# Kernel optimization log

Measured on AMD Instinct MI355X. Metric: run time of the kernel, lower is better.

## Reference

```python
import jax, jax.numpy as jnp
import numpy as np
import math

B, S, D = 4, 4096, 1024
NUM_HEADS = 8  # hardcoded in the original via `// 8` and view(..., 8, head_dim)
HEAD_DIM = D // NUM_HEADS


def setup_inputs() -> dict:
    key = jax.random.key(0)
    ks = jax.random.split(key, 11)
    s = 1.0 / math.sqrt(D)
    inp = {
        "input_seq": jax.random.normal(ks[0], (B, S, D), dtype=jnp.float32),
        # Linear weights stored as [in, out] (y = x @ W + b), matching nn.Linear math
        "Wq": jax.random.uniform(ks[1], (D, D), jnp.float32, -s, s),
        "bq": jax.random.uniform(ks[2], (D,), jnp.float32, -s, s),
        "Wk": jax.random.uniform(ks[3], (D, D), jnp.float32, -s, s),
        "bk": jax.random.uniform(ks[4], (D,), jnp.float32, -s, s),
        "Wv": jax.random.uniform(ks[5], (D, D), jnp.float32, -s, s),
        "bv": jax.random.uniform(ks[6], (D,), jnp.float32, -s, s),
        "W1": jax.random.uniform(ks[7], (D, D), jnp.float32, -s, s),
        "b1": jax.random.uniform(ks[8], (D,), jnp.float32, -s, s),
        "W2": jax.random.uniform(ks[9], (D, D), jnp.float32, -s, s),
        "b2": jax.random.uniform(ks[10], (D,), jnp.float32, -s, s),
    }
    return inp


def reference(input_seq, Wq, bq, Wk, bk, Wv, bv, W1, b1, W2, b2):
    # QKV projections (query=key=input_seq in self-attention)
    q = input_seq @ Wq + bq  # [B,S,D]
    k = input_seq @ Wk + bk
    v = input_seq @ Wv + bv

    # Faithful to the original: view(B, S, 8, head_dim) with NO transpose,
    # so attention is computed over the 8 heads within each token position.
    q = q.reshape(B, S, NUM_HEADS, HEAD_DIM)
    k = k.reshape(B, S, NUM_HEADS, HEAD_DIM)
    v = v.reshape(B, S, NUM_HEADS, HEAD_DIM)

    # scores[b,s,h,t] = q[b,s,h,:] . k[b,s,t,:] / sqrt(head_dim)  -> [B,S,8,8]
    scores = jnp.einsum("bshd,bstd->bsht", q, k) / jnp.sqrt(jnp.float32(HEAD_DIM))
    # dropout on scores before softmax: identity at inference
    attn_weights = jax.nn.softmax(scores, axis=-1)  # [B,S,8,8]

    out = jnp.einsum("bsht,bstd->bshd", attn_weights, v).reshape(B, S, D)
    # dropout on attn_output: identity at inference

    # FFN: Linear -> ReLU -> Linear (no residual / layernorm in the original)
    ff = jnp.maximum(out @ W1 + b1, 0.0) @ W2 + b2
    return ff, attn_weights
```

## Files before the change

kernel.cpp:

```cpp
#include <hip/hip_runtime.h>
#include <hip/hip_bf16.h>


#define DI __device__ __forceinline__

typedef __bf16 bf16raw;
typedef bf16raw bf16x8 __attribute__((ext_vector_type(8)));
typedef float floatx4 __attribute__((ext_vector_type(4)));

DI unsigned short f2bf(float f) {
    __hip_bfloat16 h = __float2bfloat16(f);
    return *reinterpret_cast<unsigned short*>(&h);
}

DI void async16(unsigned short* lds, const unsigned short* g) {
    __builtin_amdgcn_global_load_lds(
        (const __attribute__((address_space(1))) void*)g,
        (__attribute__((address_space(3))) void*)lds,
        16, 0, 0);
}

template <typename T> DI T cvt_out(float v);
template <> DI float cvt_out<float>(float v) { return v; }
template <> DI unsigned short cvt_out<unsigned short>(float v) { return f2bf(v); }

template <int K, int N, int GX, typename OutT, bool RELU>
__global__ __launch_bounds__(256, 3)
void gemm_bt_kernel(const unsigned short* __restrict__ A,
                    const unsigned short* __restrict__ Bt,
                    const float* __restrict__ bias,
                    OutT* __restrict__ C)
{
    constexpr int BM = 128, BN = 128, BK = 64;
    __shared__ unsigned short As[BM * BK];
    __shared__ unsigned short Bs[BN * BK];

    const int tid  = threadIdx.x;
    const int wave = tid >> 6;
    const int lane = tid & 63;
    const int quad = lane >> 4;
    const int l16  = lane & 15;
    const int sw7  = l16 & 7;

    const int g   = blockIdx.x + GX * blockIdx.y;
    const int xcd = g & 7;
    const int t   = g >> 3;
    const int bx  = t % GX;
    const int by  = t / GX + (gridDim.y >> 3) * xcd;

    const int m0 = by * BM;
    const int n0 = bx * BN;
    const int wm = (wave >> 1) * 64;
    const int wn = (wave & 1) * 64;

    floatx4 acc[4][4];
    const floatx4 zero = {0.f, 0.f, 0.f, 0.f};
#pragma unroll
    for (int i = 0; i < 4; i++)
#pragma unroll
        for (int j = 0; j < 4; j++) acc[i][j] = zero;

    const int rA = lane >> 3;
    const int kA = (((lane & 7) ^ rA) * 8);
    const unsigned short* aBase = A  + (size_t)(m0 + wave * 32 + rA) * K + kA;
    const unsigned short* bBase = Bt + (size_t)(n0 + wave * 32 + rA) * K + kA;
    unsigned short* aD = &As[wave * 2048];
    unsigned short* bD = &Bs[wave * 2048];

    for (int kt = 0; kt < K; kt += BK) {
        __syncthreads();
#pragma unroll
        for (int c = 0; c < 4; c++) {
            async16(aD + c * 512, aBase + c * 8 * K + kt);
            async16(bD + c * 512, bBase + c * 8 * K + kt);
        }
        __syncthreads();

#pragma unroll
        for (int s = 0; s < 2; s++) {
            bf16x8 af[4], bfr[4];
            const int slot = ((s * 4 + quad) ^ sw7) * 8;
#pragma unroll
            for (int i = 0; i < 4; i++)
                af[i] = *reinterpret_cast<const bf16x8*>(
                    &As[(wm + i * 16 + l16) * BK + slot]);
#pragma unroll
            for (int j = 0; j < 4; j++)
                bfr[j] = *reinterpret_cast<const bf16x8*>(
                    &Bs[(wn + j * 16 + l16) * BK + slot]);
#pragma unroll
            for (int i = 0; i < 4; i++)
#pragma unroll
                for (int j = 0; j < 4; j++)
                    acc[i][j] = __builtin_amdgcn_mfma_f32_16x16x32_bf16(
                        af[i], bfr[j], acc[i][j], 0, 0, 0);
        }
    }

#pragma unroll
    for (int j = 0; j < 4; j++) {
        const int col = n0 + wn + j * 16 + l16;
        const float bv = bias[col];
#pragma unroll
        for (int i = 0; i < 4; i++) {
            const int rbase = m0 + wm + i * 16 + quad * 4;
#pragma unroll
            for (int r = 0; r < 4; r++) {
                float v = acc[i][j][r] + bv;
                if (RELU) v = fmaxf(v, 0.f);
                C[(size_t)(rbase + r) * N + col] = cvt_out<OutT>(v);
            }
        }
    }
}

__global__ void cast_f32_to_bf16(const float* __restrict__ src,
                                 unsigned short* __restrict__ dst, int n4) {
    int i = blockIdx.x * blockDim.x + threadIdx.x;
    if (i < n4) {
        float4 v = reinterpret_cast<const float4*>(src)[i];
        ushort4 o = { f2bf(v.x), f2bf(v.y), f2bf(v.z), f2bf(v.w) };
        reinterpret_cast<ushort4*>(dst)[i] = o;
    }
}

struct WPack {
    const float* src[5];
    unsigned short* dst[5];
};
__global__ void transpose_cast_all(WPack p) {
    __shared__ float tile[32][33];
    const float* W = p.src[blockIdx.z];
    unsigned short* Wt = p.dst[blockIdx.z];
    const int n0 = blockIdx.x * 32, k0 = blockIdx.y * 32;
    const int tx = threadIdx.x, ty = threadIdx.y;
#pragma unroll
    for (int i = 0; i < 32; i += 8)
        tile[ty + i][tx] = W[(size_t)(k0 + ty + i) * 1024 + n0 + tx];
    __syncthreads();
#pragma unroll
    for (int i = 0; i < 32; i += 8)
        Wt[(size_t)(n0 + ty + i) * 1024 + k0 + tx] = f2bf(tile[tx][ty + i]);
}

__global__ void concat_bias(const float* __restrict__ bq,
                            const float* __restrict__ bk,
                            const float* __restrict__ bv,
                            float* __restrict__ dst) {
    int i = blockIdx.x * blockDim.x + threadIdx.x;
    const float* s = (i < 1024) ? bq : ((i < 2048) ? bk : bv);
    dst[i] = s[i & 1023];
}

DI float dot8(unsigned a, unsigned b, float acc) {
    union { unsigned u; float f; } al, ah, bl, bh;
    al.u = a << 16; ah.u = a & 0xffff0000u;
    bl.u = b << 16; bh.u = b & 0xffff0000u;
    return acc + al.f * bl.f + ah.f * bh.f;
}

__global__ __launch_bounds__(256)
void attention_kernel(const unsigned short* __restrict__ qkv,
                      unsigned short* __restrict__ out_bf,
                      float* __restrict__ attn_w)
{
    __shared__ unsigned short sqkv[4][3072];
    __shared__ float sw[4][64];
    const int tid  = threadIdx.x;
    const int wave = tid >> 6;
    const int lane = tid & 63;
    const int m    = blockIdx.x * 4 + wave;

    {
        const uint4* src = reinterpret_cast<const uint4*>(qkv + (size_t)m * 3072);
        uint4* dst = reinterpret_cast<uint4*>(&sqkv[wave][0]);
#pragma unroll
        for (int i = 0; i < 6; i++) dst[lane + 64 * i] = src[lane + 64 * i];
    }
    __syncthreads();

    {
        const int h = lane >> 3, t = lane & 7;
        const uint2* q8 = reinterpret_cast<const uint2*>(&sqkv[wave][h * 128]);
        const uint2* k8 = reinterpret_cast<const uint2*>(&sqkv[wave][1024 + t * 128]);
        float dot = 0.f;
#pragma unroll
        for (int d = 0; d < 32; d++) {
            uint2 a = q8[d], b = k8[d];
            dot = dot8(a.x, b.x, dot);
            dot = dot8(a.y, b.y, dot);
        }
        float score = dot * 0.08838834764831843f;
        float mx = score;
#pragma unroll
        for (int o = 1; o < 8; o <<= 1) mx = fmaxf(mx, __shfl_xor(mx, o, 8));
        float e = __expf(score - mx);
        float sum = e;
#pragma unroll
        for (int o = 1; o < 8; o <<= 1) sum += __shfl_xor(sum, o, 8);
        float w = e / sum;
        sw[wave][lane] = w;
        attn_w[(size_t)m * 64 + lane] = w;
    }
    __syncthreads();

    {
        const int h  = lane >> 3;
        const int d0 = (lane & 7) * 16;
        float acc[16];
#pragma unroll
        for (int i = 0; i < 16; i++) acc[i] = 0.f;
#pragma unroll
        for (int t = 0; t < 8; t++) {
            const float w = sw[wave][h * 8 + t];
            const uint4* v8 = reinterpret_cast<const uint4*>(
                &sqkv[wave][2048 + t * 128 + d0]);
            uint4 v0 = v8[0], v1 = v8[1];
            unsigned vv[8] = { v0.x, v0.y, v0.z, v0.w, v1.x, v1.y, v1.z, v1.w };
#pragma unroll
            for (int i = 0; i < 8; i++) {
                union { unsigned u; float f; } lo, hi;
                lo.u = vv[i] << 16; hi.u = vv[i] & 0xffff0000u;
                acc[i * 2]     += w * lo.f;
                acc[i * 2 + 1] += w * hi.f;
            }
        }
        unsigned o[8];
#pragma unroll
        for (int i = 0; i < 8; i++)
            o[i] = (unsigned)f2bf(acc[i * 2]) | ((unsigned)f2bf(acc[i * 2 + 1]) << 16);
        uint4* dst = reinterpret_cast<uint4*>(out_bf + (size_t)m * 1024 + lane * 16);
        dst[0] = make_uint4(o[0], o[1], o[2], o[3]);
        dst[1] = make_uint4(o[4], o[5], o[6], o[7]);
    }
}

extern "C" void kernel_launch(void* const* d_in, const int* in_sizes, int n_in,
                              void* d_out, int out_size, void* d_ws, size_t ws_size,
                              hipStream_t stream) {
    const float* x  = (const float*)d_in[0];
    const float* Wq = (const float*)d_in[1];
    const float* bq = (const float*)d_in[2];
    const float* Wk = (const float*)d_in[3];
    const float* bk = (const float*)d_in[4];
    const float* Wv = (const float*)d_in[5];
    const float* bv = (const float*)d_in[6];
    const float* W1 = (const float*)d_in[7];
    const float* b1 = (const float*)d_in[8];
    const float* W2 = (const float*)d_in[9];
    const float* b2 = (const float*)d_in[10];

    constexpr int D = 1024;
    constexpr int M = 4 * 4096;
    constexpr size_t XN = (size_t)M * D;

    float* ff_out   = (float*)d_out;
    float* attn_out = (float*)d_out + XN;

    char* ws = (char*)d_ws;
    size_t off = 0;
    auto alloc = [&](size_t bytes) -> char* {
        char* p = ws + off;
        off += (bytes + 255) & ~(size_t)255;
        return p;
    };
    unsigned short* Xbf   = (unsigned short*)alloc(XN * 2);
    unsigned short* Wtqkv = (unsigned short*)alloc((size_t)3 * D * D * 2);
    unsigned short* Wt1   = (unsigned short*)alloc((size_t)D * D * 2);
    unsigned short* Wt2   = (unsigned short*)alloc((size_t)D * D * 2);
    float*          bqkv  = (float*)alloc(3 * D * 4);
    unsigned short* outbf = (unsigned short*)alloc(XN * 2);
    unsigned short* hbf   = (unsigned short*)alloc(XN * 2);
    unsigned short* qkv   = (unsigned short*)alloc((size_t)M * 3 * D * 2);

    cast_f32_to_bf16<<<(int)(XN / 4 / 256), 256, 0, stream>>>(x, Xbf, (int)(XN / 4));
    WPack p;
    p.src[0] = Wq; p.dst[0] = Wtqkv;
    p.src[1] = Wk; p.dst[1] = Wtqkv + (size_t)D * D;
    p.src[2] = Wv; p.dst[2] = Wtqkv + (size_t)2 * D * D;
    p.src[3] = W1; p.dst[3] = Wt1;
    p.src[4] = W2; p.dst[4] = Wt2;
    transpose_cast_all<<<dim3(32, 32, 5), dim3(32, 8), 0, stream>>>(p);
    concat_bias<<<12, 256, 0, stream>>>(bq, bk, bv, bqkv);

    gemm_bt_kernel<D, 3 * D, 24, unsigned short, false>
        <<<dim3(24, 128), 256, 0, stream>>>(Xbf, Wtqkv, bqkv, qkv);
    attention_kernel<<<M / 4, 256, 0, stream>>>(qkv, outbf, attn_out);

    gemm_bt_kernel<D, D, 8, unsigned short, true>
        <<<dim3(8, 128), 256, 0, stream>>>(outbf, Wt1, b1, hbf);
    gemm_bt_kernel<D, D, 8, float, false>
        <<<dim3(8, 128), 256, 0, stream>>>(hbf, Wt2, b2, ff_out);
}
```

Baseline: 393.7 us.

## Replace GEMM with 256x256 double-buffered pipelined kernel using 8 waves

Swaps the 128x128 single-buffered GEMM for a 256x256-tile, 512-thread kernel. It double-buffers LDS, interleaves async global-to-LDS stages with MFMA phases under explicit barriers, vmcnt waits and setprio, and splits each wave's work into four sub-tiles. The aim is to hide global load latency behind compute and raise operand reuse per tile. In exchange it uses far more LDS and registers, and the grids shrink (768 and 256 blocks), which may leave CUs unevenly loaded for the D×D GEMMs.

```diff
diff --git a/kernel.cpp b/kernel.cpp
--- a/kernel.cpp
+++ b/kernel.cpp
@@ -24,16 +24,56 @@
 template <> DI float cvt_out<float>(float v) { return v; }
 template <> DI unsigned short cvt_out<unsigned short>(float v) { return f2bf(v); }
 
+template <int I0, int J0>
+DI void mfma16(floatx4 (&acc)[8][4], const bf16x8 (&af)[4][2],
+               const bf16x8 (&bf)[2][2]) {
+#pragma unroll
+    for (int s = 0; s < 2; s++)
+#pragma unroll
+        for (int i = 0; i < 4; i++)
+#pragma unroll
+            for (int j = 0; j < 2; j++)
+                acc[I0 + i][J0 + j] = __builtin_amdgcn_mfma_f32_16x16x32_bf16(
+                    af[i][s], bf[j][s], acc[I0 + i][J0 + j], 0, 0, 0);
+}
+
+#define STG_A(b, rb, kt) do { \
+    async16(&As[b][(rb) * 64 + wofs], aS + (size_t)(rb) * K + (kt)); \
+    async16(&As[b][((rb) + 64) * 64 + wofs], aS + (size_t)((rb) + 64) * K + (kt)); \
+} while (0)
+#define STG_B(b, rb, kt) do { \
+    async16(&Bs[b][(rb) * 64 + wofs], bS + (size_t)(rb) * K + (kt)); \
+    async16(&Bs[b][((rb) + 64) * 64 + wofs], bS + (size_t)((rb) + 64) * K + (kt)); \
+} while (0)
+#define LDA4(dst, b, base) do { _Pragma("unroll") \
+    for (int i_ = 0; i_ < 4; i_++) { \
+        dst[i_][0] = *reinterpret_cast<const bf16x8*>(&As[b][(base) + i_ * 1024 + sl0]); \
+        dst[i_][1] = *reinterpret_cast<const bf16x8*>(&As[b][(base) + i_ * 1024 + sl1]); \
+    } } while (0)
+#define LDB4(dst, b, base) do { _Pragma("unroll") \
+    for (int j_ = 0; j_ < 2; j_++) { \
+        dst[j_][0] = *reinterpret_cast<const bf16x8*>(&Bs[b][(base) + j_ * 1024 + sl0]); \
+        dst[j_][1] = *reinterpret_cast<const bf16x8*>(&Bs[b][(base) + j_ * 1024 + sl1]); \
+    } } while (0)
+#define BARRIER __builtin_amdgcn_s_barrier()
+#define WAIT_LGKM0 do { asm volatile("s_waitcnt lgkmcnt(0)" ::: "memory"); \
+    __builtin_amdgcn_sched_barrier(0); } while (0)
+#define VMCNT6 asm volatile("s_waitcnt vmcnt(6)" ::: "memory")
+
 template <int K, int N, int GX, typename OutT, bool RELU>
-__global__ __launch_bounds__(256, 3)
-void gemm_bt_kernel(const unsigned short* __restrict__ A,
-                    const unsigned short* __restrict__ Bt,
-                    const float* __restrict__ bias,
-                    OutT* __restrict__ C)
+__global__ __launch_bounds__(512, 2)
+void gemm256_bt(const unsigned short* __restrict__ A,
+                const unsigned short* __restrict__ Bt,
+                const float* __restrict__ bias,
+                OutT* __restrict__ C)
 {
-    constexpr int BM = 128, BN = 128, BK = 64;
-    __shared__ unsigned short As[BM * BK];
-    __shared__ unsigned short Bs[BN * BK];
+    constexpr int BK = 64;
+    constexpr int NT = K / BK;
+    constexpr int NP = NT / 2;
+    static_assert(NT % 2 == 0 && N % 256 == 0, "");
+
+    __shared__ unsigned short As[2][256 * BK];
+    __shared__ unsigned short Bs[2][256 * BK];
 
     const int tid  = threadIdx.x;
     const int wave = tid >> 6;
@@ -41,78 +81,139 @@
     const int quad = lane >> 4;
     const int l16  = lane & 15;
     const int sw7  = l16 & 7;
+    const int wm   = wave >> 2;
+    const int wn   = wave & 3;
 
     const int g   = blockIdx.x + GX * blockIdx.y;
     const int xcd = g & 7;
     const int t   = g >> 3;
     const int bx  = t % GX;
     const int by  = t / GX + (gridDim.y >> 3) * xcd;
-
-    const int m0 = by * BM;
-    const int n0 = bx * BN;
-    const int wm = (wave >> 1) * 64;
-    const int wn = (wave & 1) * 64;
-
-    floatx4 acc[4][4];
+    const int m0  = by * 256;
+    const int n0  = bx * 256;
+
+    const int srow = tid >> 3;
+    const int soct = ((tid & 7) ^ (srow & 7)) * 8;
+    const unsigned short* aS = A  + (size_t)(m0 + srow) * K + soct;
+    const unsigned short* bS = Bt + (size_t)(n0 + srow) * K + soct;
+    const int wofs = wave * 512;
+
+    const int aro = (wm * 64 + l16) * 64;
+    const int bro = (wn * 32 + l16) * 64;
+    const int sl0 = (quad ^ sw7) * 8;
+    const int sl1 = ((quad + 4) ^ sw7) * 8;
+
+    floatx4 acc[8][4];
     const floatx4 zero = {0.f, 0.f, 0.f, 0.f};
 #pragma unroll
-    for (int i = 0; i < 4; i++)
+    for (int i = 0; i < 8; i++)
 #pragma unroll
         for (int j = 0; j < 4; j++) acc[i][j] = zero;
 
-    const int rA = lane >> 3;
-    const int kA = (((lane & 7) ^ rA) * 8);
-    const unsigned short* aBase = A  + (size_t)(m0 + wave * 32 + rA) * K + kA;
-    const unsigned short* bBase = Bt + (size_t)(n0 + wave * 32 + rA) * K + kA;
-    unsigned short* aD = &As[wave * 2048];
-    unsigned short* bD = &Bs[wave * 2048];
-
-    for (int kt = 0; kt < K; kt += BK) {
-        __syncthreads();
-#pragma unroll
-        for (int c = 0; c < 4; c++) {
-            async16(aD + c * 512, aBase + c * 8 * K + kt);
-            async16(bD + c * 512, bBase + c * 8 * K + kt);
-        }
-        __syncthreads();
-
-#pragma unroll
-        for (int s = 0; s < 2; s++) {
-            bf16x8 af[4], bfr[4];
-            const int slot = ((s * 4 + quad) ^ sw7) * 8;
-#pragma unroll
-            for (int i = 0; i < 4; i++)
-                af[i] = *reinterpret_cast<const bf16x8*>(
-                    &As[(wm + i * 16 + l16) * BK + slot]);
-#pragma unroll
-            for (int j = 0; j < 4; j++)
-                bfr[j] = *reinterpret_cast<const bf16x8*>(
-                    &Bs[(wn + j * 16 + l16) * BK + slot]);
-#pragma unroll
-            for (int i = 0; i < 4; i++)
-#pragma unroll
-                for (int j = 0; j < 4; j++)
-                    acc[i][j] = __builtin_amdgcn_mfma_f32_16x16x32_bf16(
-                        af[i], bfr[j], acc[i][j], 0, 0, 0);
-        }
-    }
+    bf16x8 a0[4][2], a1[4][2], b0[2][2], b1[2][2];
+
+    STG_A(0, 0, 0); STG_B(0, 0, 0); STG_B(0, 128, 0); STG_A(0, 128, 0);
+    STG_A(1, 0, BK); STG_B(1, 0, BK); STG_B(1, 128, BK);
+    VMCNT6;
+    BARRIER;
+
+    for (int it = 0; it < NP; ++it) {
+        const int ktA = (2 * it + 1) * BK;
+        const int kt2 = ((2 * it + 2) < NT ? (2 * it + 2) : (NT - 1)) * BK;
+        const int kt3 = ((2 * it + 3) < NT ? (2 * it + 3) : (NT - 1)) * BK;
+
+        LDA4(a0, 0, aro);
+        LDB4(b0, 0, bro);
+        STG_A(1, 128, ktA);
+        BARRIER; WAIT_LGKM0;
+        __builtin_amdgcn_s_setprio(1);
+        mfma16<0, 0>(acc, a0, b0);
+        __builtin_amdgcn_s_setprio(0);
+        BARRIER;
+
+        LDB4(b1, 0, bro + 8192);
+        STG_A(0, 0, kt2);
+        BARRIER; WAIT_LGKM0;
+        __builtin_amdgcn_s_setprio(1);
+        mfma16<0, 2>(acc, a0, b1);
+        __builtin_amdgcn_s_setprio(0);
+        BARRIER;
+
+        LDA4(a1, 0, aro + 8192);
+        STG_B(0, 0, kt2);
+        BARRIER; WAIT_LGKM0;
+        __builtin_amdgcn_s_setprio(1);
+        mfma16<4, 0>(acc, a1, b0);
+        __builtin_amdgcn_s_setprio(0);
+        BARRIER;
+
+        STG_B(0, 128, kt2);
+        VMCNT6;
+        BARRIER;
+        __builtin_amdgcn_s_setprio(1);
+        mfma16<4, 2>(acc, a1, b1);
+        __builtin_amdgcn_s_setprio(0);
+        BARRIER;
+
+        LDA4(a0, 1, aro);
+        LDB4(b0, 1, bro);
+        STG_A(0, 128, kt2);
+        BARRIER; WAIT_LGKM0;
+        __builtin_amdgcn_s_setprio(1);
+        mfma16<0, 0>(acc, a0, b0);
+        __builtin_amdgcn_s_setprio(0);
+        BARRIER;
+
+        LDB4(b1, 1, bro + 8192);
+        STG_A(1, 0, kt3);
+        BARRIER; WAIT_LGKM0;
+        __builtin_amdgcn_s_setprio(1);
+        mfma16<0, 2>(acc, a0, b1);
+        __builtin_amdgcn_s_setprio(0);
+        BARRIER;
+
+        LDA4(a1, 1, aro + 8192);
+        STG_B(1, 0, kt3);
+        BARRIER; WAIT_LGKM0;
+        __builtin_amdgcn_s_setprio(1);
+        mfma16<4, 0>(acc, a1, b0);
+        __builtin_amdgcn_s_setprio(0);
+        BARRIER;
+
+        STG_B(1, 128, kt3);
+        VMCNT6;
+        BARRIER;
+        __builtin_amdgcn_s_setprio(1);
+        mfma16<4, 2>(acc, a1, b1);
+        __builtin_amdgcn_s_setprio(0);
+        BARRIER;
+    }
+    asm volatile("s_waitcnt vmcnt(0)" ::: "memory");
 
 #pragma unroll
     for (int j = 0; j < 4; j++) {
-        const int col = n0 + wn + j * 16 + l16;
+        const int col = n0 + wn * 32 + (j & 1) * 16 + (j >> 1) * 128 + l16;
         const float bv = bias[col];
 #pragma unroll
-        for (int i = 0; i < 4; i++) {
-            const int rbase = m0 + wm + i * 16 + quad * 4;
+        for (int i = 0; i < 8; i++) {
+            const int rb = m0 + wm * 64 + (i & 3) * 16 + (i >> 2) * 128 + quad * 4;
 #pragma unroll
             for (int r = 0; r < 4; r++) {
                 float v = acc[i][j][r] + bv;
                 if (RELU) v = fmaxf(v, 0.f);
-                C[(size_t)(rbase + r) * N + col] = cvt_out<OutT>(v);
+                C[(size_t)(rb + r) * N + col] = cvt_out<OutT>(v);
             }
         }
     }
 }
+
+#undef STG_A
+#undef STG_B
+#undef LDA4
+#undef LDB4
+#undef BARRIER
+#undef WAIT_LGKM0
+#undef VMCNT6
 
 __global__ void cast_f32_to_bf16(const float* __restrict__ src,
                                  unsigned short* __restrict__ dst, int n4) {
@@ -283,12 +384,12 @@
     transpose_cast_all<<<dim3(32, 32, 5), dim3(32, 8), 0, stream>>>(p);
     concat_bias<<<12, 256, 0, stream>>>(bq, bk, bv, bqkv);
 
-    gemm_bt_kernel<D, 3 * D, 24, unsigned short, false>
-        <<<dim3(24, 128), 256, 0, stream>>>(Xbf, Wtqkv, bqkv, qkv);
+    gemm256_bt<D, 3 * D, 12, unsigned short, false>
+        <<<dim3(12, 64), 512, 0, stream>>>(Xbf, Wtqkv, bqkv, qkv);
     attention_kernel<<<M / 4, 256, 0, stream>>>(qkv, outbf, attn_out);
 
-    gemm_bt_kernel<D, D, 8, unsigned short, true>
-        <<<dim3(8, 128), 256, 0, stream>>>(outbf, Wt1, b1, hbf);
-    gemm_bt_kernel<D, D, 8, float, false>
-        <<<dim3(8, 128), 256, 0, stream>>>(hbf, Wt2, b2, ff_out);
-}
+    gemm256_bt<D, D, 4, unsigned short, true>
+        <<<dim3(4, 64), 512, 0, stream>>>(outbf, Wt1, b1, hbf);
+    gemm256_bt<D, D, 4, float, false>
+        <<<dim3(4, 64), 512, 0, stream>>>(hbf, Wt2, b2, ff_out);
+}
```

Measured after the change: 371.2 us. 1.06x faster.
